# Performance work log

Hardware: AMD Instinct MI355X
Metric: run time of the kernel (lower is better)

Reference implementation:

```python
import jax, jax.numpy as jnp
import numpy as np

NHID = 512
T_K, T_Q, B = 256, 128, 8


def setup_inputs() -> dict:
    key = jax.random.key(0)
    k1, k2, k3, k4, k5 = jax.random.split(key, 5)
    query = jax.random.normal(k1, (T_Q, B, NHID), dtype=jnp.float32)
    c_key = jax.random.normal(k2, (T_K, B, NHID), dtype=jnp.float32)
    mask = jax.random.randint(k3, (T_K, B), 0, 2).astype(bool)
    # att_mlp params: Linear(2*nhid, nhid) -> Tanh -> Linear(nhid, 1)
    # stored as [in, out] so y = x @ W + b (torch Linear weight transposed)
    W1 = jax.random.normal(k4, (2 * NHID, NHID), dtype=jnp.float32) / np.sqrt(2 * NHID)
    b1 = jnp.zeros((NHID,), dtype=jnp.float32)
    W2 = jax.random.normal(k5, (NHID, 1), dtype=jnp.float32) / np.sqrt(NHID)
    b2 = jnp.zeros((1,), dtype=jnp.float32)
    return {"query": query, "c_key": c_key, "mask": mask,
            "W1": W1, "b1": b1, "W2": W2, "b2": b2}


def reference(query, c_key, mask, W1, b1, W2, b2):
    H = query.shape[-1]
    # cat([k_expand, q_expand], -1) @ W1 == k @ W1[:H] + q @ W1[H:]
    # (avoids materializing the [T_k, T_q, B, 2H] concat the torch code builds)
    k_proj = jnp.einsum('kbh,hd->kbd', c_key, W1[:H])   # [T_k, B, H]
    q_proj = jnp.einsum('qbh,hd->qbd', query, W1[H:])   # [T_q, B, H]
    h = jnp.tanh(k_proj[:, None, :, :] + q_proj[None, :, :, :] + b1)  # [T_k, T_q, B, H]
    att_score = jnp.einsum('kqbh,ho->kqb', h, W2) + b2[0]             # [T_k, T_q, B]
    att_score = jnp.where(mask[:, None, :], -jnp.inf, att_score)
    att_prob = jax.nn.softmax(att_score, axis=0)                      # softmax over keys
    # c_val defaults to c_key in the original forward
    ant_vec = jnp.einsum('kqb,kbh->qbh', att_prob, c_key)             # [T_q, B, H]
    return ant_vec, att_prob
```

## Files before the change

kernel.cpp:

```cpp
#include <hip/hip_runtime.h>
#include <math.h>

#define NHID 512
#define T_K  256
#define T_Q  128
#define BB   8

constexpr float C2L2E = 2.8853900817779268f;
constexpr float L2E   = 1.4426950408889634f;

__device__ __forceinline__ float fexp2(float x) { return __builtin_amdgcn_exp2f(x); }
__device__ __forceinline__ float frcp(float x)  { return __builtin_amdgcn_rcpf(x); }

typedef __attribute__((ext_vector_type(8))) short bf16x8;
typedef __attribute__((ext_vector_type(4))) float f32x4;

__device__ __forceinline__ unsigned short f2bf(float x) {
    unsigned u = __builtin_bit_cast(unsigned, x);
    unsigned r = (u + 0x7FFFu + ((u >> 16) & 1u)) >> 16;
    return (unsigned short)r;
}
__device__ __forceinline__ float bf2f(unsigned short h) {
    unsigned u = ((unsigned)h) << 16;
    return __builtin_bit_cast(float, u);
}
__device__ __forceinline__ unsigned packbf(float a, float b) {
    return (unsigned)f2bf(a) | ((unsigned)f2bf(b) << 16);
}
__device__ __forceinline__ float lo16(unsigned u) {
    return __builtin_bit_cast(float, u << 16);
}
__device__ __forceinline__ float hi16(unsigned u) {
    return __builtin_bit_cast(float, u & 0xFFFF0000u);
}

__global__ __launch_bounds__(256) void convert_kernel(
    const float* __restrict__ W1, const float* __restrict__ ckey,
    unsigned short* __restrict__ bt_hi, unsigned short* __restrict__ bt_lo,
    unsigned int* __restrict__ ckp)
{
    const int bid = blockIdx.x;
    const int t   = threadIdx.x;
    if (bid < 128) {
        const int kt = bid & 15;
        const int nt = bid >> 4;
        __shared__ float tile[64][65];
        const int r  = t >> 2;
        const int c0 = (t & 3) * 16;
        const float* src = W1 + (size_t)(kt * 64 + r) * 512 + nt * 64 + c0;
        #pragma unroll
        for (int j = 0; j < 4; ++j) {
            const float4 v = *(const float4*)&src[j * 4];
            tile[r][c0 + j * 4 + 0] = v.x; tile[r][c0 + j * 4 + 1] = v.y;
            tile[r][c0 + j * 4 + 2] = v.z; tile[r][c0 + j * 4 + 3] = v.w;
        }
        __syncthreads();
        const size_t dst = (size_t)((kt >> 3) * 512 + nt * 64 + r) * 512
                         + (size_t)((kt & 7) * 64 + c0);
        #pragma unroll
        for (int j4 = 0; j4 < 4; ++j4) {
            ushort4 h, l;
            #pragma unroll
            for (int e = 0; e < 4; ++e) {
                const float x = tile[c0 + j4 * 4 + e][r];
                const unsigned short hb = f2bf(x);
                ((unsigned short*)&h)[e] = hb;
                ((unsigned short*)&l)[e] = f2bf(x - bf2f(hb));
            }
            *(ushort4*)&bt_hi[dst + j4 * 4] = h;
            *(ushort4*)&bt_lo[dst + j4 * 4] = l;
        }
    } else {
        const int cb = bid - 128;
        const int b  = cb >> 5;
        const int kt = cb & 31;
        const int kloc = t >> 5;
        const int g    = t & 31;
        const int k = kt * 8 + kloc;
        const float* src = ckey + ((size_t)k * 8 + b) * 512 + g * 16;
        const float4 v0 = *(const float4*)&src[0];
        const float4 v1 = *(const float4*)&src[4];
        const float4 v2 = *(const float4*)&src[8];
        const float4 v3 = *(const float4*)&src[12];
        uint4 o0, o1;
        o0.x = packbf(v0.x, v0.y); o0.y = packbf(v0.z, v0.w);
        o0.z = packbf(v1.x, v1.y); o0.w = packbf(v1.z, v1.w);
        o1.x = packbf(v2.x, v2.y); o1.y = packbf(v2.z, v2.w);
        o1.z = packbf(v3.x, v3.y); o1.w = packbf(v3.z, v3.w);
        unsigned int* dst = ckp + ((size_t)b * 256 + k) * 256 + g * 8;
        *(uint4*)&dst[0] = o0;
        *(uint4*)&dst[4] = o1;
    }
}

__global__ __launch_bounds__(256) void proj_kernel(
    const float* __restrict__ qry, const float* __restrict__ ckey,
    const unsigned short* __restrict__ bt_hi, const unsigned short* __restrict__ bt_lo,
    const float* __restrict__ b1,
    uint2* __restrict__ ektq, float* __restrict__ eq)
{
    const int row0 = blockIdx.x * 32;
    const int col0 = blockIdx.y * 64;
    const bool isK = row0 < 2048;
    const int bhalf = isK ? 0 : 512;

    __shared__ __align__(16) unsigned short As_h[32 * 64];
    __shared__ __align__(16) unsigned short As_l[32 * 64];
    __shared__ __align__(16) unsigned short Bs_h[64 * 64];
    __shared__ __align__(16) unsigned short Bs_l[64 * 64];

    const int t    = threadIdx.x;
    const int wave = t >> 6;
    const int lane = t & 63;
    const int wm = (wave & 1) * 16;
    const int wn = (wave >> 1) * 32;

    f32x4 acc[2] = {};

    const int srA = t >> 3;
    const int scA = (t & 7) * 8;
    const float* gA = (isK ? ckey + (size_t)(row0 + srA) * 512
                           : qry  + (size_t)(row0 - 2048 + srA) * 512) + scA;
    const int swA = ((scA >> 3) ^ (srA & 7)) * 8;

    const int srB = t >> 2;
    const int scB = (t & 3) * 16;
    const unsigned short* gBh = bt_hi + (size_t)(bhalf + col0 + srB) * 512 + scB;
    const unsigned short* gBl = bt_lo + (size_t)(bhalf + col0 + srB) * 512 + scB;
    const int cB = scB >> 3;
    const int swB0 = ((cB + 0) ^ (srB & 7)) * 8;
    const int swB1 = ((cB + 1) ^ (srB & 7)) * 8;

    const int quad = lane >> 4, fr = lane & 15;

    float4 pa0 = *(const float4*)&gA[0];
    float4 pa1 = *(const float4*)&gA[4];
    uint4  pbh0 = *(const uint4*)&gBh[0], pbh1 = *(const uint4*)&gBh[8];
    uint4  pbl0 = *(const uint4*)&gBl[0], pbl1 = *(const uint4*)&gBl[8];

    for (int k0 = 0; k0 < 512; k0 += 64) {
        float fa[8];
        *(float4*)&fa[0] = pa0; *(float4*)&fa[4] = pa1;
        union { uint4 v; unsigned short s[8]; } h0, l0;
        #pragma unroll
        for (int e = 0; e < 8; ++e) {
            const unsigned short hb = f2bf(fa[e]);
            h0.s[e] = hb; l0.s[e] = f2bf(fa[e] - bf2f(hb));
        }
        __syncthreads();
        *(uint4*)&As_h[srA * 64 + swA] = h0.v;
        *(uint4*)&As_l[srA * 64 + swA] = l0.v;
        *(uint4*)&Bs_h[srB * 64 + swB0] = pbh0; *(uint4*)&Bs_h[srB * 64 + swB1] = pbh1;
        *(uint4*)&Bs_l[srB * 64 + swB0] = pbl0; *(uint4*)&Bs_l[srB * 64 + swB1] = pbl1;
        __syncthreads();

        if (k0 + 64 < 512) {
            pa0 = *(const float4*)&gA[k0 + 64];
            pa1 = *(const float4*)&gA[k0 + 68];
            pbh0 = *(const uint4*)&gBh[k0 + 64]; pbh1 = *(const uint4*)&gBh[k0 + 72];
            pbl0 = *(const uint4*)&gBl[k0 + 64]; pbl1 = *(const uint4*)&gBl[k0 + 72];
        }

        #pragma unroll
        for (int ks = 0; ks < 2; ++ks) {
            const int cchunk = ks * 4 + quad;
            const int m = wm + fr;
            const bf16x8 afh = *(const bf16x8*)&As_h[m * 64 + ((cchunk ^ (m & 7)) * 8)];
            const bf16x8 afl = *(const bf16x8*)&As_l[m * 64 + ((cchunk ^ (m & 7)) * 8)];
            bf16x8 bfh[2], bfl[2];
            #pragma unroll
            for (int nt = 0; nt < 2; ++nt) {
                const int n = wn + nt * 16 + fr;
                bfh[nt] = *(const bf16x8*)&Bs_h[n * 64 + ((cchunk ^ (n & 7)) * 8)];
                bfl[nt] = *(const bf16x8*)&Bs_l[n * 64 + ((cchunk ^ (n & 7)) * 8)];
            }
            #pragma unroll
            for (int nt = 0; nt < 2; ++nt) {
                acc[nt] = __builtin_amdgcn_mfma_f32_16x16x32_bf16(afh, bfh[nt], acc[nt], 0, 0, 0);
                acc[nt] = __builtin_amdgcn_mfma_f32_16x16x32_bf16(afh, bfl[nt], acc[nt], 0, 0, 0);
                acc[nt] = __builtin_amdgcn_mfma_f32_16x16x32_bf16(afl, bfh[nt], acc[nt], 0, 0, 0);
            }
        }
    }

    #pragma unroll
    for (int nt = 0; nt < 2; ++nt) {
        const int colg = col0 + wn + nt * 16 + fr;
        const float b1v = b1[colg];
        #pragma unroll
        for (int i = 0; i < 4; ++i) {
            const int rowg = row0 + wm + quad * 4 + i;
            const float v = acc[nt][i];
            if (isK) {
                const float e = fexp2((v + b1v) * C2L2E);
                const float ep = __shfl_xor(e, 1, 64);
                unsigned pk = ((fr & 1) == 0) ? packbf(e, ep) : packbf(ep, e);
                const unsigned pk2 = __shfl_xor(pk, 2, 64);
                if ((fr & 3) == 0) {
                    const int kidx = rowg >> 3;
                    const int bb   = rowg & 7;
                    const int hq   = colg >> 2;
                    ektq[((size_t)bb * 128 + hq) * 256 + kidx] = make_uint2(pk, pk2);
                }
            } else {
                eq[(size_t)(rowg - 2048) * 512 + colg] = fexp2(v * C2L2E);
            }
        }
    }
}

__global__ __launch_bounds__(512) void scoreav_kernel(
    const uint2* __restrict__ ektq, const float* __restrict__ eq,
    const float* __restrict__ W2, const float* __restrict__ b2,
    const int* __restrict__ mask, const unsigned int* __restrict__ ckp,
    float* __restrict__ prob_out, float* __restrict__ out_ant)
{
    const int t    = threadIdx.x;
    const int lane = t & 63;
    const int wave = __builtin_amdgcn_readfirstlane(t >> 6);
    const int kk   = t & 255;
    const int half = t >> 8;
    const int q0   = blockIdx.x * 2;
    const int b    = blockIdx.y;

    __shared__ float eq0s[512], eq1s[512], w2s[512];
    __shared__ float rp[2][512];
    __shared__ float ps[2][256];

    eq0s[t] = eq[((size_t)q0 * 8 + b) * 512 + t];
    eq1s[t] = eq[((size_t)(q0 + 1) * 8 + b) * 512 + t];
    w2s[t]  = W2[t];

    const float4 wA = *(const float4*)&W2[lane * 4];
    const float4 wB = *(const float4*)&W2[256 + lane * 4];
    float s2 = wA.x + wA.y + wA.z + wA.w + wB.x + wB.y + wB.z + wB.w;
    #pragma unroll
    for (int m = 32; m; m >>= 1) s2 += __shfl_xor(s2, m, 64);
    const float base = s2 + b2[0];
    __syncthreads();

    const uint2* __restrict__ ekb = ektq + (size_t)b * 128 * 256 + kk;
    float r0a = 0.f, r0b = 0.f, r1a = 0.f, r1b = 0.f;

    uint2 L[2][8];
    #pragma unroll
    for (int j = 0; j < 8; ++j)
        L[0][j] = ekb[(size_t)(half * 64 + j) * 256];

    for (int g = 0; g < 8; ++g) {
        const int cur = g & 1;
        if (g < 7) {
            #pragma unroll
            for (int j = 0; j < 8; ++j)
                L[cur ^ 1][j] = ekb[(size_t)(half * 64 + (g + 1) * 8 + j) * 256];
        }
        #pragma unroll
        for (int j = 0; j < 8; ++j) {
            const int h = (half * 64 + g * 8 + j) * 4;
            const float ek0 = lo16(L[cur][j].x);
            const float ek1 = hi16(L[cur][j].x);
            const float ek2 = lo16(L[cur][j].y);
            const float ek3 = hi16(L[cur][j].y);
            const float4 w  = *(const float4*)&w2s[h];
            const float4 e0 = *(const float4*)&eq0s[h];
            const float4 e1 = *(const float4*)&eq1s[h];
            {
                const float a0 = fmaf(ek0, e0.x, 1.0f);
                const float a1 = fmaf(ek1, e0.y, 1.0f);
                const float a2 = fmaf(ek2, e0.z, 1.0f);
                const float a3 = fmaf(ek3, e0.w, 1.0f);
                const float d01 = a0 * a1, d23 = a2 * a3;
                const float n01 = fmaf(w.x, a1, w.y * a0);
                const float n23 = fmaf(w.z, a3, w.w * a2);
                const float N = fmaf(n01, d23, n23 * d01);
                if (j & 1) r0b = fmaf(N, frcp(d01 * d23), r0b);
                else       r0a = fmaf(N, frcp(d01 * d23), r0a);
            }
            {
                const float a0 = fmaf(ek0, e1.x, 1.0f);
                const float a1 = fmaf(ek1, e1.y, 1.0f);
                const float a2 = fmaf(ek2, e1.z, 1.0f);
                const float a3 = fmaf(ek3, e1.w, 1.0f);
                const float d01 = a0 * a1, d23 = a2 * a3;
                const float n01 = fmaf(w.x, a1, w.y * a0);
                const float n23 = fmaf(w.z, a3, w.w * a2);
                const float N = fmaf(n01, d23, n23 * d01);
                if (j & 1) r1b = fmaf(N, frcp(d01 * d23), r1b);
                else       r1a = fmaf(N, frcp(d01 * d23), r1a);
            }
        }
    }
    rp[0][t] = r0a + r0b;
    rp[1][t] = r1a + r1b;
    __syncthreads();

    if (t < 256) {
        const int msk = mask[t * 8 + b];
        float s0 = base - 2.0f * (rp[0][t] + rp[0][t + 256]);
        float s1 = base - 2.0f * (rp[1][t] + rp[1][t + 256]);
        if (msk) { s0 = -INFINITY; s1 = -INFINITY; }
        ps[0][t] = s0;
        ps[1][t] = s1;
    }
    __syncthreads();

    if (wave < 2) {
        float4 sv = *(const float4*)&ps[wave][lane * 4];
        float m = fmaxf(fmaxf(sv.x, sv.y), fmaxf(sv.z, sv.w));
        #pragma unroll
        for (int d = 32; d; d >>= 1) m = fmaxf(m, __shfl_xor(m, d, 64));
        float4 pv;
        pv.x = fexp2((sv.x - m) * L2E);
        pv.y = fexp2((sv.y - m) * L2E);
        pv.z = fexp2((sv.z - m) * L2E);
        pv.w = fexp2((sv.w - m) * L2E);
        float sum = pv.x + pv.y + pv.z + pv.w;
        #pragma unroll
        for (int d = 32; d; d >>= 1) sum += __shfl_xor(sum, d, 64);
        const float inv = frcp(sum);
        pv.x *= inv; pv.y *= inv; pv.z *= inv; pv.w *= inv;
        *(float4*)&ps[wave][lane * 4] = pv;
        const int qb_idx = (q0 + wave) * 8 + b;
        const int kbase = lane * 4;
        prob_out[(size_t)(kbase + 0) * 1024 + qb_idx] = pv.x;
        prob_out[(size_t)(kbase + 1) * 1024 + qb_idx] = pv.y;
        prob_out[(size_t)(kbase + 2) * 1024 + qb_idx] = pv.z;
        prob_out[(size_t)(kbase + 3) * 1024 + qb_idx] = pv.w;
    }
    __syncthreads();

    {
        const int kq  = lane >> 4;
        const int hq2 = lane & 15;
        const int pbase = wave * 32 + hq2 * 2;
        const unsigned int* __restrict__ ckb = ckp + (size_t)b * 256 * 256;
        float4 a0 = {}, a1 = {};
        #pragma unroll 8
        for (int ki = 0; ki < 64; ++ki) {
            const int k = ki * 4 + kq;
            const uint2 U = *(const uint2*)&ckb[(size_t)k * 256 + pbase];
            const float c0 = lo16(U.x), c1 = hi16(U.x);
            const float c2 = lo16(U.y), c3 = hi16(U.y);
            const float p0 = ps[0][k];
            const float p1 = ps[1][k];
            a0.x = fmaf(p0, c0, a0.x); a0.y = fmaf(p0, c1, a0.y);
            a0.z = fmaf(p0, c2, a0.z); a0.w = fmaf(p0, c3, a0.w);
            a1.x = fmaf(p1, c0, a1.x); a1.y = fmaf(p1, c1, a1.y);
            a1.z = fmaf(p1, c2, a1.z); a1.w = fmaf(p1, c3, a1.w);
        }
        #pragma unroll
        for (int d = 16; d <= 32; d <<= 1) {
            a0.x += __shfl_xor(a0.x, d, 64); a0.y += __shfl_xor(a0.y, d, 64);
            a0.z += __shfl_xor(a0.z, d, 64); a0.w += __shfl_xor(a0.w, d, 64);
            a1.x += __shfl_xor(a1.x, d, 64); a1.y += __shfl_xor(a1.y, d, 64);
            a1.z += __shfl_xor(a1.z, d, 64); a1.w += __shfl_xor(a1.w, d, 64);
        }
        if (lane < 32) {
            const int qi = kq & 1;
            const int h0 = wave * 64 + hq2 * 4;
            const float4 outv = (qi == 0) ? a0 : a1;
            *(float4*)&out_ant[((size_t)(q0 + qi) * 8 + b) * 512 + h0] = outv;
        }
    }
}

extern "C" void kernel_launch(void* const* d_in, const int* in_sizes, int n_in,
                              void* d_out, int out_size, void* d_ws, size_t ws_size,
                              hipStream_t stream)
{
    const float* qry  = (const float*)d_in[0];
    const float* ckey = (const float*)d_in[1];
    const int*   mask = (const int*)d_in[2];
    const float* W1   = (const float*)d_in[3];
    const float* b1   = (const float*)d_in[4];
    const float* W2   = (const float*)d_in[5];
    const float* b2   = (const float*)d_in[6];

    float* out_ant  = (float*)d_out;
    float* out_prob = (float*)d_out + T_Q * BB * NHID;

    float* ws = (float*)d_ws;
    uint2* ws_ektq = (uint2*)ws;
    float* ws_eq  = ws + 524288;
    unsigned short* bt_hi = (unsigned short*)(ws + 1048576);
    unsigned short* bt_lo = (unsigned short*)(ws + 1310720);
    unsigned int* ws_ckp  = (unsigned int*)(ws + 1572864);

    convert_kernel<<<dim3(384), 256, 0, stream>>>(W1, ckey, bt_hi, bt_lo, ws_ckp);
    proj_kernel<<<dim3(96, 8), 256, 0, stream>>>(qry, ckey, bt_hi, bt_lo, b1, ws_ektq, ws_eq);
    scoreav_kernel<<<dim3(64, 8), 512, 0, stream>>>(ws_ektq, ws_eq, W2, b2, mask, ws_ckp,
                                                    out_prob, out_ant);
}
```

Measured before the change: 111.4 us.

## Fuse W1 and c_key bf16 conversion into projection kernel, drop convert pass

Removes the separate convert kernel. The projection kernel now reads fp32 W1 directly, splits it into hi/lo bf16 in registers, and stores it transposed into shared memory. The col0==0 key blocks also emit the packed bf16 c_key copy that the score kernel needs. This saves one launch and the round trip of the converted weights through global memory. In exchange, every projection block redoes the W1 conversion, and the W1 reads become strided scalar loads.

```diff
diff --git a/kernel.cpp b/kernel.cpp
--- a/kernel.cpp
+++ b/kernel.cpp
@@ -34,70 +34,11 @@
     return __builtin_bit_cast(float, u & 0xFFFF0000u);
 }
 
-__global__ __launch_bounds__(256) void convert_kernel(
-    const float* __restrict__ W1, const float* __restrict__ ckey,
-    unsigned short* __restrict__ bt_hi, unsigned short* __restrict__ bt_lo,
-    unsigned int* __restrict__ ckp)
-{
-    const int bid = blockIdx.x;
-    const int t   = threadIdx.x;
-    if (bid < 128) {
-        const int kt = bid & 15;
-        const int nt = bid >> 4;
-        __shared__ float tile[64][65];
-        const int r  = t >> 2;
-        const int c0 = (t & 3) * 16;
-        const float* src = W1 + (size_t)(kt * 64 + r) * 512 + nt * 64 + c0;
-        #pragma unroll
-        for (int j = 0; j < 4; ++j) {
-            const float4 v = *(const float4*)&src[j * 4];
-            tile[r][c0 + j * 4 + 0] = v.x; tile[r][c0 + j * 4 + 1] = v.y;
-            tile[r][c0 + j * 4 + 2] = v.z; tile[r][c0 + j * 4 + 3] = v.w;
-        }
-        __syncthreads();
-        const size_t dst = (size_t)((kt >> 3) * 512 + nt * 64 + r) * 512
-                         + (size_t)((kt & 7) * 64 + c0);
-        #pragma unroll
-        for (int j4 = 0; j4 < 4; ++j4) {
-            ushort4 h, l;
-            #pragma unroll
-            for (int e = 0; e < 4; ++e) {
-                const float x = tile[c0 + j4 * 4 + e][r];
-                const unsigned short hb = f2bf(x);
-                ((unsigned short*)&h)[e] = hb;
-                ((unsigned short*)&l)[e] = f2bf(x - bf2f(hb));
-            }
-            *(ushort4*)&bt_hi[dst + j4 * 4] = h;
-            *(ushort4*)&bt_lo[dst + j4 * 4] = l;
-        }
-    } else {
-        const int cb = bid - 128;
-        const int b  = cb >> 5;
-        const int kt = cb & 31;
-        const int kloc = t >> 5;
-        const int g    = t & 31;
-        const int k = kt * 8 + kloc;
-        const float* src = ckey + ((size_t)k * 8 + b) * 512 + g * 16;
-        const float4 v0 = *(const float4*)&src[0];
-        const float4 v1 = *(const float4*)&src[4];
-        const float4 v2 = *(const float4*)&src[8];
-        const float4 v3 = *(const float4*)&src[12];
-        uint4 o0, o1;
-        o0.x = packbf(v0.x, v0.y); o0.y = packbf(v0.z, v0.w);
-        o0.z = packbf(v1.x, v1.y); o0.w = packbf(v1.z, v1.w);
-        o1.x = packbf(v2.x, v2.y); o1.y = packbf(v2.z, v2.w);
-        o1.z = packbf(v3.x, v3.y); o1.w = packbf(v3.z, v3.w);
-        unsigned int* dst = ckp + ((size_t)b * 256 + k) * 256 + g * 8;
-        *(uint4*)&dst[0] = o0;
-        *(uint4*)&dst[4] = o1;
-    }
-}
-
 __global__ __launch_bounds__(256) void proj_kernel(
     const float* __restrict__ qry, const float* __restrict__ ckey,
-    const unsigned short* __restrict__ bt_hi, const unsigned short* __restrict__ bt_lo,
-    const float* __restrict__ b1,
-    uint2* __restrict__ ektq, float* __restrict__ eq)
+    const float* __restrict__ W1, const float* __restrict__ b1,
+    uint2* __restrict__ ektq, float* __restrict__ eq,
+    unsigned int* __restrict__ ckp)
 {
     const int row0 = blockIdx.x * 32;
     const int col0 = blockIdx.y * 64;
@@ -122,43 +63,63 @@
     const float* gA = (isK ? ckey + (size_t)(row0 + srA) * 512
                            : qry  + (size_t)(row0 - 2048 + srA) * 512) + scA;
     const int swA = ((scA >> 3) ^ (srA & 7)) * 8;
-
-    const int srB = t >> 2;
-    const int scB = (t & 3) * 16;
-    const unsigned short* gBh = bt_hi + (size_t)(bhalf + col0 + srB) * 512 + scB;
-    const unsigned short* gBl = bt_lo + (size_t)(bhalf + col0 + srB) * 512 + scB;
-    const int cB = scB >> 3;
-    const int swB0 = ((cB + 0) ^ (srB & 7)) * 8;
-    const int swB1 = ((cB + 1) ^ (srB & 7)) * 8;
+    const bool emit_ckp = isK && (col0 == 0);
+    const int rowA = row0 + srA;
+    unsigned int* ckp_dst = emit_ckp
+        ? ckp + ((size_t)(rowA & 7) * 256 + (rowA >> 3)) * 256
+        : nullptr;
+
+    const int nB = t & 63;
+    const int kgB = wave * 16;
+    const float* gB = W1 + (size_t)(bhalf + kgB) * 512 + col0 + nB;
+    const int caB = wave * 2;
+    const int swB0 = nB * 64 + (((caB + 0) ^ (nB & 7)) * 8);
+    const int swB1 = nB * 64 + (((caB + 1) ^ (nB & 7)) * 8);
 
     const int quad = lane >> 4, fr = lane & 15;
 
     float4 pa0 = *(const float4*)&gA[0];
     float4 pa1 = *(const float4*)&gA[4];
-    uint4  pbh0 = *(const uint4*)&gBh[0], pbh1 = *(const uint4*)&gBh[8];
-    uint4  pbl0 = *(const uint4*)&gBl[0], pbl1 = *(const uint4*)&gBl[8];
+    float bv[16];
+    #pragma unroll
+    for (int kk = 0; kk < 16; ++kk)
+        bv[kk] = gB[(size_t)kk * 512];
 
     for (int k0 = 0; k0 < 512; k0 += 64) {
         float fa[8];
         *(float4*)&fa[0] = pa0; *(float4*)&fa[4] = pa1;
-        union { uint4 v; unsigned short s[8]; } h0, l0;
+        union { uint4 v; unsigned short s[8]; } hA, lA, bh0, bh1, bl0, bl1;
         #pragma unroll
         for (int e = 0; e < 8; ++e) {
             const unsigned short hb = f2bf(fa[e]);
-            h0.s[e] = hb; l0.s[e] = f2bf(fa[e] - bf2f(hb));
-        }
+            hA.s[e] = hb; lA.s[e] = f2bf(fa[e] - bf2f(hb));
+        }
+        #pragma unroll
+        for (int e = 0; e < 8; ++e) {
+            const unsigned short hb = f2bf(bv[e]);
+            bh0.s[e] = hb; bl0.s[e] = f2bf(bv[e] - bf2f(hb));
+        }
+        #pragma unroll
+        for (int e = 0; e < 8; ++e) {
+            const unsigned short hb = f2bf(bv[8 + e]);
+            bh1.s[e] = hb; bl1.s[e] = f2bf(bv[8 + e] - bf2f(hb));
+        }
+        if (emit_ckp)
+            *(uint4*)&ckp_dst[(k0 + scA) >> 1] = hA.v;
+
         __syncthreads();
-        *(uint4*)&As_h[srA * 64 + swA] = h0.v;
-        *(uint4*)&As_l[srA * 64 + swA] = l0.v;
-        *(uint4*)&Bs_h[srB * 64 + swB0] = pbh0; *(uint4*)&Bs_h[srB * 64 + swB1] = pbh1;
-        *(uint4*)&Bs_l[srB * 64 + swB0] = pbl0; *(uint4*)&Bs_l[srB * 64 + swB1] = pbl1;
+        *(uint4*)&As_h[srA * 64 + swA] = hA.v;
+        *(uint4*)&As_l[srA * 64 + swA] = lA.v;
+        *(uint4*)&Bs_h[swB0] = bh0.v;  *(uint4*)&Bs_h[swB1] = bh1.v;
+        *(uint4*)&Bs_l[swB0] = bl0.v;  *(uint4*)&Bs_l[swB1] = bl1.v;
         __syncthreads();
 
         if (k0 + 64 < 512) {
             pa0 = *(const float4*)&gA[k0 + 64];
             pa1 = *(const float4*)&gA[k0 + 68];
-            pbh0 = *(const uint4*)&gBh[k0 + 64]; pbh1 = *(const uint4*)&gBh[k0 + 72];
-            pbl0 = *(const uint4*)&gBl[k0 + 64]; pbl1 = *(const uint4*)&gBl[k0 + 72];
+            #pragma unroll
+            for (int kk = 0; kk < 16; ++kk)
+                bv[kk] = gB[(size_t)(k0 + 64 + kk) * 512];
         }
 
         #pragma unroll
@@ -382,12 +343,10 @@
     float* ws = (float*)d_ws;
     uint2* ws_ektq = (uint2*)ws;
     float* ws_eq  = ws + 524288;
-    unsigned short* bt_hi = (unsigned short*)(ws + 1048576);
-    unsigned short* bt_lo = (unsigned short*)(ws + 1310720);
-    unsigned int* ws_ckp  = (unsigned int*)(ws + 1572864);
-
-    convert_kernel<<<dim3(384), 256, 0, stream>>>(W1, ckey, bt_hi, bt_lo, ws_ckp);
-    proj_kernel<<<dim3(96, 8), 256, 0, stream>>>(qry, ckey, bt_hi, bt_lo, b1, ws_ektq, ws_eq);
+    unsigned int* ws_ckp = (unsigned int*)(ws + 1048576);
+
+    proj_kernel<<<dim3(96, 8), 256, 0, stream>>>(qry, ckey, W1, b1,
+                                                 ws_ektq, ws_eq, ws_ckp);
     scoreav_kernel<<<dim3(64, 8), 512, 0, stream>>>(ws_ektq, ws_eq, W2, b2, mask, ws_ckp,
                                                     out_prob, out_ant);
 }
```

Result: no change. 111.7 us (+0.3%).
